# Kernel optimization log

Measured on AMD Instinct MI355X. Metric: run time of the kernel, lower is better.

Reference implementation:

```python
import jax, jax.numpy as jnp
import numpy as np

B, S, H = 4, 2048, 2048
NH, NKV, HD = 16, 4, 128  # heads, kv heads, head_dim; group g = NH // NKV = 4
ROPE_BASE = 10000.0


def rotate_half(x):
    x1, x2 = jnp.split(x, 2, axis=-1)
    return jnp.concatenate([-x2, x1], axis=-1)


def setup_inputs() -> dict:
    key = jax.random.key(0)
    k1, k2, k3 = jax.random.split(key, 3)
    hidden_states = jax.random.normal(k1, (B, S, H), dtype=jnp.float32)
    # additive causal mask [B, 1, S, S]: 0 on/below diagonal, large negative above
    causal = jnp.tril(jnp.ones((S, S), dtype=bool))
    attention_mask = jnp.where(causal, 0.0, -1e9).astype(jnp.float32)
    attention_mask = jnp.broadcast_to(attention_mask[None, None], (B, 1, S, S))
    # RoPE tables [S, HD]
    inv_freq = 1.0 / (ROPE_BASE ** (np.arange(0, HD, 2, dtype=np.float32) / HD))
    pos = np.arange(S, dtype=np.float32)
    freqs = np.outer(pos, inv_freq)                       # [S, HD/2]
    emb = np.concatenate([freqs, freqs], axis=-1)         # [S, HD]
    rope_cos = jnp.asarray(np.cos(emb), dtype=jnp.float32)
    rope_sin = jnp.asarray(np.sin(emb), dtype=jnp.float32)
    w_attn = jax.random.normal(k2, (H, H + 2 * NKV * HD), dtype=jnp.float32) * 0.02
    w_proj = jax.random.normal(k3, (H, H), dtype=jnp.float32) * 0.02
    return {"hidden_states": hidden_states, "attention_mask": attention_mask,
            "rope_cos": rope_cos, "rope_sin": rope_sin,
            "w_attn": w_attn, "w_proj": w_proj}


def reference(hidden_states, attention_mask, rope_cos, rope_sin, w_attn, w_proj):
    g = NH // NKV
    qkv = jnp.einsum('bsh,hf->bsf', hidden_states, w_attn)          # [B,S,(g+2)*NKV*HD]
    qkv = qkv.reshape(B, S, NKV, (g + 2) * HD)
    q, k, v = jnp.split(qkv, [g * HD, (g + 1) * HD], axis=-1)
    q = q.reshape(B, S, NH, HD).transpose(0, 2, 1, 3)               # [B,NH,S,HD]
    k = k.transpose(0, 2, 1, 3)                                     # [B,NKV,S,HD]
    v = v.transpose(0, 2, 1, 3)                                     # [B,NKV,S,HD]
    cos = rope_cos[None, None]                                      # [1,1,S,HD]
    sin = rope_sin[None, None]
    q = q * cos + rotate_half(q) * sin
    k = k * cos + rotate_half(k) * sin
    # repeat kv heads to match query heads (repeat_interleave semantics)
    k = jnp.repeat(k, g, axis=1)                                    # [B,NH,S,HD]
    v = jnp.repeat(v, g, axis=1)
    scale = 1.0 / (HD ** 0.5)
    scores = jnp.einsum('bhqd,bhkd->bhqk', q, k) * scale + attention_mask
    attn = jax.nn.softmax(scores.astype(jnp.float32), axis=-1).astype(q.dtype)
    out = jnp.einsum('bhqk,bhkd->bhqd', attn, v)                    # [B,NH,S,HD]
    out = out.transpose(0, 2, 1, 3).reshape(B, S, NH * HD)
    return jnp.einsum('bsh,hf->bsf', out, w_proj)
```

## Files before the change

kernel.cpp:

```cpp
#include <hip/hip_runtime.h>
#include <hip/hip_bf16.h>
#include <stdint.h>

#define B_   4
#define S_   2048
#define H_   2048
#define NH_  16
#define NKV_ 4
#define HD_  128
#define F_   3072

typedef __bf16 bf16x8 __attribute__((ext_vector_type(8)));
typedef float  f32x4  __attribute__((ext_vector_type(4)));
typedef unsigned short u16;

#define GLOAD_LDS16(gp, lp)                                                             \
  __builtin_amdgcn_global_load_lds((const __attribute__((address_space(1))) void*)(gp), \
                                   (__attribute__((address_space(3))) void*)(lp), 16, 0, 0)

__device__ __forceinline__ u16 f2bf(float f) {
  union { float f; uint32_t u; } v; v.f = f;
  uint32_t r = (v.u + 0x7FFFu + ((v.u >> 16) & 1u)) >> 16;
  return (u16)r;
}
__device__ __forceinline__ float bf2f(u16 u) {
  union { uint32_t u; float f; } v; v.u = ((uint32_t)u) << 16;
  return v.f;
}

__global__ void k_cvt_bf16(const float* __restrict__ in, u16* __restrict__ out, int n4) {
  int i = blockIdx.x * 256 + threadIdx.x;
  if (i >= n4) return;
  float4 v = ((const float4*)in)[i];
  union { u16 s[4]; uint2 u; } o;
  o.s[0] = f2bf(v.x); o.s[1] = f2bf(v.y); o.s[2] = f2bf(v.z); o.s[3] = f2bf(v.w);
  ((uint2*)out)[i] = o.u;
}

__global__ void k_transpose_cvt(const float* __restrict__ in, u16* __restrict__ out, int R, int C) {
  __shared__ u16 tile[64][68];
  int c0 = blockIdx.x * 64, r0 = blockIdx.y * 64;
  int t = threadIdx.x;
#pragma unroll
  for (int j = 0; j < 16; ++j) {
    int e = j * 256 + t;
    int r = e >> 6, c = e & 63;
    tile[r][c] = f2bf(in[(size_t)(r0 + r) * C + (c0 + c)]);
  }
  __syncthreads();
#pragma unroll
  for (int j = 0; j < 16; ++j) {
    int e = j * 256 + t;
    int c = e >> 6, r = e & 63;
    out[(size_t)(c0 + c) * R + (r0 + r)] = tile[r][c];
  }
}

template <bool OUTF32>
__global__ __launch_bounds__(256) void k_gemm_bt(const u16* __restrict__ A, const u16* __restrict__ BT,
                                                 void* __restrict__ Cv, int M, int N, int K) {
  __shared__ u16 lA[2][128 * 64];
  __shared__ u16 lB[2][128 * 64];
  int t = threadIdx.x, w = t >> 6, l = t & 63, c = l & 15, g = l >> 4;
  int bn = blockIdx.x * 128, bm = blockIdx.y * 128;
  int wm = (w >> 1) * 64, wn = (w & 1) * 64;

  f32x4 acc[4][4];
#pragma unroll
  for (int mi = 0; mi < 4; ++mi)
#pragma unroll
    for (int ni = 0; ni < 4; ++ni) acc[mi][ni] = (f32x4){0.f, 0.f, 0.f, 0.f};

  int nk = K >> 6;
  int srow = l >> 3;
  int scol = ((l & 7) ^ srow) * 8;

#define GEMM_STAGE(k0, buf)                                                     \
  _Pragma("unroll")                                                             \
  for (int i = 0; i < 4; ++i) {                                                 \
    int ch = i * 4 + w; int row = ch * 8 + srow;                                \
    GLOAD_LDS16(&A [(size_t)(bm + row) * K + (k0) + scol], &lA[buf][ch * 512]); \
    GLOAD_LDS16(&BT[(size_t)(bn + row) * K + (k0) + scol], &lB[buf][ch * 512]); \
  }

  GEMM_STAGE(0, 0)
  asm volatile("s_waitcnt vmcnt(0)" ::: "memory");
  __syncthreads();
  int cur = 0;
  for (int kt = 0; kt < nk; ++kt) {
    if (kt + 1 < nk) { GEMM_STAGE((kt + 1) << 6, cur ^ 1) }
    const u16* cA = lA[cur];
    const u16* cB = lB[cur];
#pragma unroll
    for (int s = 0; s < 2; ++s) {
      bf16x8 af[4], bfr[4];
#pragma unroll
      for (int mi = 0; mi < 4; ++mi) {
        int row = wm + mi * 16 + c;
        af[mi] = *(const bf16x8*)&cA[row * 64 + (((s * 4 + g) ^ (c & 7)) * 8)];
      }
#pragma unroll
      for (int ni = 0; ni < 4; ++ni) {
        int row = wn + ni * 16 + c;
        bfr[ni] = *(const bf16x8*)&cB[row * 64 + (((s * 4 + g) ^ (c & 7)) * 8)];
      }
#pragma unroll
      for (int mi = 0; mi < 4; ++mi)
#pragma unroll
        for (int ni = 0; ni < 4; ++ni)
          acc[mi][ni] = __builtin_amdgcn_mfma_f32_16x16x32_bf16(af[mi], bfr[ni], acc[mi][ni], 0, 0, 0);
    }
    if (kt + 1 < nk) {
      asm volatile("s_waitcnt vmcnt(0)" ::: "memory");
      __syncthreads();
      cur ^= 1;
    }
  }
#pragma unroll
  for (int mi = 0; mi < 4; ++mi)
#pragma unroll
    for (int ni = 0; ni < 4; ++ni)
#pragma unroll
      for (int r = 0; r < 4; ++r) {
        size_t row = (size_t)bm + wm + mi * 16 + 4 * g + r;
        size_t col = (size_t)bn + wn + ni * 16 + c;
        if constexpr (OUTF32) ((float*)Cv)[row * N + col] = acc[mi][ni][r];
        else                  ((u16*)Cv)  [row * N + col] = f2bf(acc[mi][ni][r]);
      }
#undef GEMM_STAGE
}

__global__ void k_rope_qk(const u16* __restrict__ qkv, const float* __restrict__ ct,
                          const float* __restrict__ st, u16* __restrict__ Q, u16* __restrict__ Kd) {
  size_t idx = (size_t)blockIdx.x * 256 + threadIdx.x;
  const size_t NQ = (size_t)B_ * NH_ * S_ * HD_;
  int d, s, row, col; size_t oidx; u16* dst;
  if (idx < NQ) {
    d = (int)(idx & 127); s = (int)((idx >> 7) & (S_ - 1));
    int h = (int)((idx >> 18) & 15); int b = (int)(idx >> 22);
    row = b * S_ + s;
    col = (h >> 2) * 768 + (h & 3) * 128 + d;
    dst = Q; oidx = idx;
  } else {
    size_t i2 = idx - NQ;
    d = (int)(i2 & 127); s = (int)((i2 >> 7) & (S_ - 1));
    int kvh = (int)((i2 >> 18) & 3); int b = (int)(i2 >> 20);
    row = b * S_ + s;
    col = kvh * 768 + 512 + d;
    dst = Kd; oidx = i2;
  }
  float x  = bf2f(qkv[(size_t)row * F_ + col]);
  float xr = (d < 64) ? -bf2f(qkv[(size_t)row * F_ + col + 64])
                      :  bf2f(qkv[(size_t)row * F_ + col - 64]);
  float o = x * ct[s * HD_ + d] + xr * st[s * HD_ + d];
  dst[oidx] = f2bf(o);
}

__global__ void k_transpose_v(const u16* __restrict__ qkv, u16* __restrict__ Vt) {
  __shared__ u16 tile[64][136];
  int s0 = blockIdx.x * 64;
  int b = blockIdx.y >> 2, kvh = blockIdx.y & 3;
  int t = threadIdx.x;
  const u16* src = qkv + (size_t)(b * S_ + s0) * F_ + kvh * 768 + 640;
#pragma unroll
  for (int j = 0; j < 4; ++j) {
    int e = j * 256 + t;
    int sl = e >> 4, ch = e & 15;
    *(uint4*)&tile[sl][ch * 8] = *(const uint4*)&src[(size_t)sl * F_ + ch * 8];
  }
  __syncthreads();
  u16* dstb = Vt + (size_t)(b * NKV_ + kvh) * HD_ * S_;
#pragma unroll
  for (int j = 0; j < 4; ++j) {
    int e = j * 256 + t;
    int d = e & 127, sc = e >> 7;
    u16 tmp[8];
#pragma unroll
    for (int i = 0; i < 8; ++i) tmp[i] = tile[sc * 8 + i][d];
    *(uint4*)&dstb[(size_t)d * S_ + s0 + sc * 8] = *(const uint4*)tmp;
  }
}

__global__ __launch_bounds__(256, 2) void k_flash(const u16* __restrict__ Q, const u16* __restrict__ K,
                                                  const u16* __restrict__ Vt, u16* __restrict__ O) {
  __shared__ u16 lK[2][64 * 128];
  __shared__ u16 lV[2][128 * 64];
  __shared__ u16 lP[4][16 * 64];
  int t = threadIdx.x, w = t >> 6, l = t & 63, c = l & 15, g = l >> 4;
  int qb = (int)(gridDim.x - 1 - blockIdx.x);
  int bh = blockIdx.y;
  int b = bh >> 4, h = bh & 15, kvh = h >> 2;
  int qw = qb * 64 + w * 16;
  const u16* Qb = Q  + (size_t)(b * NH_  + h)   * S_ * HD_;
  const u16* Kb = K  + (size_t)(b * NKV_ + kvh) * S_ * HD_;
  const u16* Vb = Vt + (size_t)(b * NKV_ + kvh) * HD_ * S_;

  bf16x8 qf[4];
#pragma unroll
  for (int sl = 0; sl < 4; ++sl)
    qf[sl] = *(const bf16x8*)&Qb[(size_t)(qw + c) * HD_ + sl * 32 + g * 8];

  f32x4 oacc[8];
#pragma unroll
  for (int nd = 0; nd < 8; ++nd) oacc[nd] = (f32x4){0.f, 0.f, 0.f, 0.f};
  float m_run = -1e30f, l_run = 0.f;

  int ntiles = qb + 1;
  int krl = l >> 4;
  int vrl = l >> 3;

#define STAGE_KV(kv0, buf)                                                           \
  _Pragma("unroll")                                                                  \
  for (int i = 0; i < 4; ++i) {                                                      \
    int ch = i * 4 + w;                                                              \
    int rrK = ch * 4 + krl;                                                          \
    int jK  = (l & 15) ^ (rrK & 15);                                                 \
    GLOAD_LDS16(&Kb[(size_t)((kv0) + rrK) * HD_ + jK * 8], &lK[buf][ch * 512]);      \
    int rdV = ch * 8 + vrl;                                                          \
    int jV  = (l & 7) ^ (rdV & 7);                                                   \
    GLOAD_LDS16(&Vb[(size_t)rdV * S_ + (kv0) + jV * 8], &lV[buf][ch * 512]);         \
  }

  STAGE_KV(0, 0)
  asm volatile("s_waitcnt vmcnt(0)" ::: "memory");
  __syncthreads();
  int cur = 0;

  for (int kt = 0; kt < ntiles; ++kt) {
    int kv0 = kt * 64;
    if (kt + 1 < ntiles) { STAGE_KV(kv0 + 64, cur ^ 1) }
    {
      const u16* cK = lK[cur];
      const u16* cV = lV[cur];
      f32x4 sc[4];
#pragma unroll
      for (int f = 0; f < 4; ++f) sc[f] = (f32x4){0.f, 0.f, 0.f, 0.f};
#pragma unroll
      for (int sl = 0; sl < 4; ++sl)
#pragma unroll
        for (int f = 0; f < 4; ++f) {
          bf16x8 kf = *(const bf16x8*)&cK[(f * 16 + c) * 128 + (((sl * 4 + g) ^ c) * 8)];
          sc[f] = __builtin_amdgcn_mfma_f32_16x16x32_bf16(kf, qf[sl], sc[f], 0, 0, 0);
        }
      const float SCL = 0.088388347648318447f * 1.4426950408889634f;
      bool partial = (kv0 + 63 > qw);
      float pvv[4][4];
      float pm = -1e30f;
#pragma unroll
      for (int f = 0; f < 4; ++f)
#pragma unroll
        for (int r = 0; r < 4; ++r) {
          float v = sc[f][r] * SCL;
          if (partial && (kv0 + f * 16 + 4 * g + r > qw + c)) v = -1e30f;
          pvv[f][r] = v;
          pm = fmaxf(pm, v);
        }
      pm = fmaxf(pm, __shfl_xor(pm, 16));
      pm = fmaxf(pm, __shfl_xor(pm, 32));
      float m_new = fmaxf(m_run, pm);
      float alpha = exp2f(m_run - m_new);
      float ps = 0.f;
#pragma unroll
      for (int f = 0; f < 4; ++f)
#pragma unroll
        for (int r = 0; r < 4; ++r) {
          float p = exp2f(pvv[f][r] - m_new);
          pvv[f][r] = p;
          ps += p;
        }
      ps += __shfl_xor(ps, 16);
      ps += __shfl_xor(ps, 32);
      l_run = l_run * alpha + ps;
      m_run = m_new;
#pragma unroll
      for (int r = 0; r < 4; ++r) {
        float ar = __shfl(alpha, 4 * g + r);
#pragma unroll
        for (int nd = 0; nd < 8; ++nd) oacc[nd][r] *= ar;
      }
      char* Pw = (char*)&lP[w][0];
#pragma unroll
      for (int f = 0; f < 4; ++f) {
        int base = f * 32 + g * 8;
        int chunk = base >> 4, within = base & 15;
        uint32_t p01 = (uint32_t)f2bf(pvv[f][0]) | ((uint32_t)f2bf(pvv[f][1]) << 16);
        uint32_t p23 = (uint32_t)f2bf(pvv[f][2]) | ((uint32_t)f2bf(pvv[f][3]) << 16);
        int rowb = c * 128 + ((chunk ^ (c & 7)) << 4) + within;
        *(uint32_t*)(Pw + rowb)     = p01;
        *(uint32_t*)(Pw + rowb + 4) = p23;
      }
#pragma unroll
      for (int ks = 0; ks < 2; ++ks) {
        bf16x8 pf = *(const bf16x8*)(Pw + c * 128 + (((ks * 4 + g) ^ (c & 7)) << 4));
#pragma unroll
        for (int nd = 0; nd < 8; ++nd) {
          int rowv = nd * 16 + c;
          bf16x8 vf = *(const bf16x8*)&cV[rowv * 64 + (((ks * 4 + g) ^ (c & 7)) * 8)];
          oacc[nd] = __builtin_amdgcn_mfma_f32_16x16x32_bf16(pf, vf, oacc[nd], 0, 0, 0);
        }
      }
    }
    if (kt + 1 < ntiles) {
      asm volatile("s_waitcnt vmcnt(0)" ::: "memory");
      __syncthreads();
      cur ^= 1;
    }
  }
#undef STAGE_KV
  float lr[4];
#pragma unroll
  for (int r = 0; r < 4; ++r) {
    float lv = __shfl(l_run, 4 * g + r);
    lr[r] = 1.f / lv;
  }
#pragma unroll
  for (int nd = 0; nd < 8; ++nd)
#pragma unroll
    for (int r = 0; r < 4; ++r) {
      size_t row = (size_t)b * S_ + (qw + 4 * g + r);
      O[row * (NH_ * HD_) + h * HD_ + nd * 16 + c] = f2bf(oacc[nd][r] * lr[r]);
    }
}

extern "C" void kernel_launch(void* const* d_in, const int* in_sizes, int n_in,
                              void* d_out, int out_size, void* d_ws, size_t ws_size,
                              hipStream_t stream) {
  const float* hid   = (const float*)d_in[0];
  const float* rcos  = (const float*)d_in[2];
  const float* rsin  = (const float*)d_in[3];
  const float* wattn = (const float*)d_in[4];
  const float* wproj = (const float*)d_in[5];

  u16* ws   = (u16*)d_ws;
  u16* hidB = ws;
  u16* wAT  = ws + 16777216;
  u16* wPT  = ws + 23068672;
  u16* qkv  = ws + 27262976;
  u16* Qs   = ws + 52428800;
  u16* Ks   = ws + 69206016;
  u16* Vts  = ws + 73400320;
  u16* Os   = qkv;

  k_cvt_bf16<<<16384, 256, 0, stream>>>(hid, hidB, 16777216 / 4);
  k_transpose_cvt<<<dim3(48, 32), 256, 0, stream>>>(wattn, wAT, 2048, 3072);
  k_transpose_cvt<<<dim3(32, 32), 256, 0, stream>>>(wproj, wPT, 2048, 2048);
  k_gemm_bt<false><<<dim3(24, 64), 256, 0, stream>>>(hidB, wAT, qkv, 8192, 3072, 2048);
  k_rope_qk<<<81920, 256, 0, stream>>>(qkv, rcos, rsin, Qs, Ks);
  k_transpose_v<<<dim3(32, 16), 256, 0, stream>>>(qkv, Vts);
  k_flash<<<dim3(32, 64), 256, 0, stream>>>(Qs, Ks, Vts, Os);
  k_gemm_bt<true><<<dim3(16, 64), 256, 0, stream>>>(Os, wPT, d_out, 8192, 2048, 2048);
}
```

Before: 673.9 us.

## Enlarge flash-attention query block to 128 rows with single-buffered KV staging

The flash kernel now uses 512-thread blocks covering 128 query rows (8 waves), halving the grid so each staged K/V tile is reused by twice as many queries. The double-buffered K/V LDS staging is replaced by a single buffer loaded and waited on each iteration, which shrinks LDS per block so more blocks can be resident. Waves whose rows lie entirely before the current KV tile skip its compute. The trade-off is that prefetch overlap is lost, adding exposed load latency and two barriers per tile, and causal work becomes less balanced within a block.

Result: slower. 743.7 us (+10.4%).

```diff
diff --git a/kernel.cpp b/kernel.cpp
--- a/kernel.cpp
+++ b/kernel.cpp
@@ -181,16 +181,16 @@
   }
 }
 
-__global__ __launch_bounds__(256, 2) void k_flash(const u16* __restrict__ Q, const u16* __restrict__ K,
+__global__ __launch_bounds__(512, 6) void k_flash(const u16* __restrict__ Q, const u16* __restrict__ K,
                                                   const u16* __restrict__ Vt, u16* __restrict__ O) {
-  __shared__ u16 lK[2][64 * 128];
-  __shared__ u16 lV[2][128 * 64];
-  __shared__ u16 lP[4][16 * 64];
+  __shared__ u16 lK[64 * 128];
+  __shared__ u16 lV[128 * 64];
+  __shared__ u16 lP[8][16 * 64];
   int t = threadIdx.x, w = t >> 6, l = t & 63, c = l & 15, g = l >> 4;
   int qb = (int)(gridDim.x - 1 - blockIdx.x);
   int bh = blockIdx.y;
   int b = bh >> 4, h = bh & 15, kvh = h >> 2;
-  int qw = qb * 64 + w * 16;
+  int qw = qb * 128 + w * 16;
   const u16* Qb = Q  + (size_t)(b * NH_  + h)   * S_ * HD_;
   const u16* Kb = K  + (size_t)(b * NKV_ + kvh) * S_ * HD_;
   const u16* Vb = Vt + (size_t)(b * NKV_ + kvh) * HD_ * S_;
@@ -205,33 +205,26 @@
   for (int nd = 0; nd < 8; ++nd) oacc[nd] = (f32x4){0.f, 0.f, 0.f, 0.f};
   float m_run = -1e30f, l_run = 0.f;
 
-  int ntiles = qb + 1;
+  int ntiles = 2 * qb + 2;
   int krl = l >> 4;
   int vrl = l >> 3;
 
-#define STAGE_KV(kv0, buf)                                                           \
-  _Pragma("unroll")                                                                  \
-  for (int i = 0; i < 4; ++i) {                                                      \
-    int ch = i * 4 + w;                                                              \
-    int rrK = ch * 4 + krl;                                                          \
-    int jK  = (l & 15) ^ (rrK & 15);                                                 \
-    GLOAD_LDS16(&Kb[(size_t)((kv0) + rrK) * HD_ + jK * 8], &lK[buf][ch * 512]);      \
-    int rdV = ch * 8 + vrl;                                                          \
-    int jV  = (l & 7) ^ (rdV & 7);                                                   \
-    GLOAD_LDS16(&Vb[(size_t)rdV * S_ + (kv0) + jV * 8], &lV[buf][ch * 512]);         \
-  }
-
-  STAGE_KV(0, 0)
-  asm volatile("s_waitcnt vmcnt(0)" ::: "memory");
-  __syncthreads();
-  int cur = 0;
-
   for (int kt = 0; kt < ntiles; ++kt) {
     int kv0 = kt * 64;
-    if (kt + 1 < ntiles) { STAGE_KV(kv0 + 64, cur ^ 1) }
-    {
-      const u16* cK = lK[cur];
-      const u16* cV = lV[cur];
+    __syncthreads();
+#pragma unroll
+    for (int i = 0; i < 2; ++i) {
+      int ch = i * 8 + w;
+      int rrK = ch * 4 + krl;
+      int jK  = (l & 15) ^ (rrK & 15);
+      GLOAD_LDS16(&Kb[(size_t)(kv0 + rrK) * HD_ + jK * 8], &lK[ch * 512]);
+      int rdV = ch * 8 + vrl;
+      int jV  = (l & 7) ^ (rdV & 7);
+      GLOAD_LDS16(&Vb[(size_t)rdV * S_ + kv0 + jV * 8], &lV[ch * 512]);
+    }
+    asm volatile("s_waitcnt vmcnt(0)" ::: "memory");
+    __syncthreads();
+    if (kv0 <= qw + 15) {
       f32x4 sc[4];
 #pragma unroll
       for (int f = 0; f < 4; ++f) sc[f] = (f32x4){0.f, 0.f, 0.f, 0.f};
@@ -239,7 +232,7 @@
       for (int sl = 0; sl < 4; ++sl)
 #pragma unroll
         for (int f = 0; f < 4; ++f) {
-          bf16x8 kf = *(const bf16x8*)&cK[(f * 16 + c) * 128 + (((sl * 4 + g) ^ c) * 8)];
+          bf16x8 kf = *(const bf16x8*)&lK[(f * 16 + c) * 128 + (((sl * 4 + g) ^ c) * 8)];
           sc[f] = __builtin_amdgcn_mfma_f32_16x16x32_bf16(kf, qf[sl], sc[f], 0, 0, 0);
         }
       const float SCL = 0.088388347648318447f * 1.4426950408889634f;
@@ -295,18 +288,12 @@
 #pragma unroll
         for (int nd = 0; nd < 8; ++nd) {
           int rowv = nd * 16 + c;
-          bf16x8 vf = *(const bf16x8*)&cV[rowv * 64 + (((ks * 4 + g) ^ (c & 7)) * 8)];
+          bf16x8 vf = *(const bf16x8*)&lV[rowv * 64 + (((ks * 4 + g) ^ (c & 7)) * 8)];
           oacc[nd] = __builtin_amdgcn_mfma_f32_16x16x32_bf16(pf, vf, oacc[nd], 0, 0, 0);
         }
       }
     }
-    if (kt + 1 < ntiles) {
-      asm volatile("s_waitcnt vmcnt(0)" ::: "memory");
-      __syncthreads();
-      cur ^= 1;
-    }
-  }
-#undef STAGE_KV
+  }
   float lr[4];
 #pragma unroll
   for (int r = 0; r < 4; ++r) {
@@ -347,6 +334,6 @@
   k_gemm_bt<false><<<dim3(24, 64), 256, 0, stream>>>(hidB, wAT, qkv, 8192, 3072, 2048);
   k_rope_qk<<<81920, 256, 0, stream>>>(qkv, rcos, rsin, Qs, Ks);
   k_transpose_v<<<dim3(32, 16), 256, 0, stream>>>(qkv, Vts);
-  k_flash<<<dim3(32, 64), 256, 0, stream>>>(Qs, Ks, Vts, Os);
+  k_flash<<<dim3(16, 64), 512, 0, stream>>>(Qs, Ks, Vts, Os);
   k_gemm_bt<true><<<dim3(16, 64), 256, 0, stream>>>(Os, wPT, d_out, 8192, 2048, 2048);
 }
```
